# Kernel tuning notes

Measured on AMD Instinct MI355X. Metric: run time of the kernel, lower is better.

Reference implementation:

```python
import jax, jax.numpy as jnp
import numpy as np

B, S, H, E, I, K = 1, 4096, 1024, 16, 512, 2
ISH = 1024  # shared expert intermediate = moe_intermediate_size * num_shared_experts
ROUTE_SCALE = 1.0
WSCALE = 0.02


def setup_inputs() -> dict:
    key = jax.random.key(0)
    ks = jax.random.split(key, 9)
    return {
        "hidden_states": jax.random.normal(ks[0], (B, S, H), dtype=jnp.float32),
        "router_w": jax.random.normal(ks[1], (H, E), dtype=jnp.float32) * WSCALE,
        "expert_bias": jnp.zeros((E,), dtype=jnp.float32),
        "w_gate": jax.random.normal(ks[2], (E, H, I), dtype=jnp.float32) * WSCALE,
        "w_up": jax.random.normal(ks[3], (E, H, I), dtype=jnp.float32) * WSCALE,
        "w_down": jax.random.normal(ks[4], (E, I, H), dtype=jnp.float32) * WSCALE,
        "sw_gate": jax.random.normal(ks[5], (H, ISH), dtype=jnp.float32) * WSCALE,
        "sw_up": jax.random.normal(ks[6], (H, ISH), dtype=jnp.float32) * WSCALE,
        "sw_down": jax.random.normal(ks[7], (ISH, H), dtype=jnp.float32) * WSCALE,
    }


def reference(hidden_states, router_w, expert_bias, w_gate, w_up, w_down, sw_gate, sw_up, sw_down):
    b, s, h = hidden_states.shape
    T = b * s
    xf = hidden_states.reshape(T, h)

    # --- token-choice router (sigmoid scores, top-k, normalize, scale) ---
    scores = jax.nn.sigmoid((xf @ router_w).astype(jnp.float32))          # [T, E]
    _, sel = jax.lax.top_k(scores + expert_bias[None, :], K)              # [T, K] int32
    top = jnp.take_along_axis(scores, sel, axis=1)                        # [T, K]
    top = top / (top.sum(axis=-1, keepdims=True) + 1e-20)
    top = top * ROUTE_SCALE

    # combine weights: [T, E], zero for unselected experts
    comb = jnp.zeros((T, E), jnp.float32).at[jnp.arange(T)[:, None], sel].add(top)

    # --- routed experts: SwiGLU MLP per expert (stacked weights) ---
    g = jnp.einsum('th,ehi->eti', xf, w_gate)                             # [E, T, I]
    u = jnp.einsum('th,ehi->eti', xf, w_up)                               # [E, T, I]
    a = jax.nn.silu(g) * u                                                # [E, T, I]
    eo = jnp.einsum('eti,eih->eth', a, w_down)                            # [E, T, H]
    routed = jnp.einsum('eth,te->th', eo.astype(jnp.float32), comb).astype(hidden_states.dtype)

    # --- shared experts (always active) ---
    shared = (jax.nn.silu(xf @ sw_gate) * (xf @ sw_up)) @ sw_down         # [T, H]

    return (shared + routed).reshape(b, s, h)
```

## Files before the change

kernel.cpp:

```cpp
#include <hip/hip_runtime.h>
#include <math.h>

#define T_TOK 4096
#define HDIM  1024
#define NEXP  16
#define IDIM  512
#define NSLOT 16384
#define NGRP  18
#define MAXRB 160

typedef unsigned int u32;
typedef unsigned short u16;
typedef __attribute__((ext_vector_type(8))) short bfrag;
typedef __attribute__((ext_vector_type(4))) float f32x4;

__device__ __forceinline__ u16 f2bf(float f) {
    union { float f; u32 u; } c; c.f = f;
    u32 u = c.u;
    u32 r = u + 0x7fffu + ((u >> 16) & 1u);
    return (u16)(r >> 16);
}
__device__ __forceinline__ float bf2f(u16 h) {
    union { u32 u; float f; } c; c.u = ((u32)h) << 16;
    return c.f;
}

__device__ __forceinline__ void async16(void* lds, const void* g) {
    __builtin_amdgcn_global_load_lds((__attribute__((address_space(1))) void*)(g),
                                     (__attribute__((address_space(3))) void*)(lds),
                                     16, 0, 0);
}

#define SYNCN(n) do { \
    asm volatile("s_waitcnt vmcnt(" #n ")" ::: "memory"); \
    __builtin_amdgcn_s_barrier(); \
    __builtin_amdgcn_sched_barrier(0); \
} while (0)
#define BAR2() do { \
    __builtin_amdgcn_s_barrier(); \
    __builtin_amdgcn_sched_barrier(0); \
} while (0)

__global__ __launch_bounds__(256)
void transpose_all_k(const float* __restrict__ wg, const float* __restrict__ wu,
                     const float* __restrict__ wd, const float* __restrict__ swg,
                     const float* __restrict__ swu, const float* __restrict__ swd,
                     u16* __restrict__ WtG, u16* __restrict__ WtU, u16* __restrict__ WtD,
                     u16* __restrict__ SWtG, u16* __restrict__ SWtU, u16* __restrict__ SWtD) {
    int z = blockIdx.z;
    const float* src; u16* dst; int R, C; long base;
    if (z < 16)      { src = wg;  dst = WtG;  R = HDIM; C = IDIM;     base = (long)z * HDIM * IDIM; }
    else if (z < 32) { src = wu;  dst = WtU;  R = HDIM; C = IDIM;     base = (long)(z - 16) * HDIM * IDIM; }
    else if (z < 48) { src = wd;  dst = WtD;  R = IDIM; C = HDIM;     base = (long)(z - 32) * IDIM * HDIM; }
    else if (z == 48){ src = swg; dst = SWtG; R = HDIM; C = 2 * IDIM; base = 0; }
    else if (z == 49){ src = swu; dst = SWtU; R = HDIM; C = 2 * IDIM; base = 0; }
    else             { src = swd; dst = SWtD; R = IDIM; C = HDIM;     base = (long)(z - 50) * IDIM * HDIM; }
    if ((int)blockIdx.x >= C / 32 || (int)blockIdx.y >= R / 128) return;

    __shared__ u16 tileT[32][132];
    int c0 = blockIdx.x * 32, r0 = blockIdx.y * 128;
    int t = threadIdx.x;
    int rr = t >> 3;
    int c4 = (t & 7) * 4;
#pragma unroll
    for (int p = 0; p < 4; ++p) {
        int r = p * 32 + rr;
        float4 v = *(const float4*)(src + base + (long)(r0 + r) * C + c0 + c4);
        tileT[c4 + 0][r] = f2bf(v.x);
        tileT[c4 + 1][r] = f2bf(v.y);
        tileT[c4 + 2][r] = f2bf(v.z);
        tileT[c4 + 3][r] = f2bf(v.w);
    }
    __syncthreads();
    int cc = t >> 5;
    int r4 = (t & 31) * 4;
#pragma unroll
    for (int q = 0; q < 4; ++q) {
        int c = q * 8 + cc;
        ushort4 o;
        o.x = tileT[c][r4]; o.y = tileT[c][r4 + 1];
        o.z = tileT[c][r4 + 2]; o.w = tileT[c][r4 + 3];
        *(ushort4*)(dst + base + (long)(c0 + c) * R + r0 + r4) = o;
    }
}

__global__ __launch_bounds__(256) void router_k(const float* __restrict__ x,
                                                const float* __restrict__ rw,
                                                const float* __restrict__ bias,
                                                int* __restrict__ sel,
                                                float* __restrict__ wts,
                                                u16* __restrict__ x_bf) {
    int tid = threadIdx.x;
    int wv = tid >> 6;
    int lane = tid & 63;
    int t = blockIdx.x * 4 + wv;

    const float4* xr4 = (const float4*)(x + (long)t * HDIM);
    ushort4* xb4 = (ushort4*)(x_bf + (long)t * HDIM);
#pragma unroll
    for (int j = 0; j < 4; ++j) {
        float4 v = xr4[lane + j * 64];
        ushort4 ov;
        ov.x = f2bf(v.x); ov.y = f2bf(v.y); ov.z = f2bf(v.z); ov.w = f2bf(v.w);
        xb4[lane + j * 64] = ov;
    }

    int e = lane & 15, hc = lane >> 4;
    const float* xr = x + (long)t * HDIM + hc * 256;
    const float* rp = rw + (long)hc * 256 * NEXP + e;
    float acc = 0.f;
#pragma unroll 4
    for (int i = 0; i < 64; ++i) {
        float4 xv = *(const float4*)(xr + i * 4);
        acc += xv.x * rp[(i * 4 + 0) * NEXP] + xv.y * rp[(i * 4 + 1) * NEXP]
             + xv.z * rp[(i * 4 + 2) * NEXP] + xv.w * rp[(i * 4 + 3) * NEXP];
    }
    acc += __shfl_down(acc, 16);
    acc += __shfl_down(acc, 32);
    float sc = 1.f / (1.f + __expf(-acc));
    float v = sc + bias[e];
    int i0 = -1, i1 = -1;
    float v0 = -1e30f, v1 = -1e30f, s0 = 0.f, s1 = 0.f;
#pragma unroll
    for (int j = 0; j < 16; ++j) {
        float vj = __shfl(v, j);
        float scj = __shfl(sc, j);
        if (vj > v0) { v1 = v0; i1 = i0; s1 = s0; v0 = vj; i0 = j; s0 = scj; }
        else if (vj > v1) { v1 = vj; i1 = j; s1 = scj; }
    }
    if (lane == 0) {
        float nrm = s0 + s1 + 1e-20f;
        sel[t * 2] = i0; sel[t * 2 + 1] = i1;
        wts[t * 2] = s0 / nrm; wts[t * 2 + 1] = s1 / nrm;
    }
}

__global__ __launch_bounds__(1024) void route_build_k(const int* __restrict__ sel,
                                                      int* __restrict__ offs,
                                                      int* __restrict__ rowmap,
                                                      int* __restrict__ invmap,
                                                      int* __restrict__ rbGroup,
                                                      int* __restrict__ rbRow0) {
    __shared__ int hist[NEXP];
    __shared__ int cur[NEXP];
    int tid = threadIdx.x;
    if (tid < NEXP) hist[tid] = 0;
    __syncthreads();
    for (int i = tid; i < T_TOK * 2; i += 1024)
        atomicAdd(&hist[sel[i]], 1);
    __syncthreads();
    if (tid == 0) {
        int a = 0;
        for (int g = 0; g < NEXP; ++g) { cur[g] = a; offs[g] = a; a += hist[g]; }
        offs[16] = 8192;
        offs[17] = 8192 + T_TOK;
        offs[18] = 8192 + 2 * T_TOK;
        int rb = 0;
        for (int g = 0; g < NGRP; ++g)
            for (int r0 = offs[g]; r0 < offs[g + 1]; r0 += 128) {
                rbGroup[rb] = g; rbRow0[rb] = r0; ++rb;
            }
        for (; rb < MAXRB; ++rb) rbGroup[rb] = -1;
    }
    __syncthreads();
    for (int i = tid; i < T_TOK * 2; i += 1024) {
        int g = sel[i];
        int slot = atomicAdd(&cur[g], 1);
        rowmap[slot] = i >> 1;
        invmap[i] = slot;
    }
    for (int i = tid; i < T_TOK; i += 1024) {
        rowmap[8192 + i] = i;
        rowmap[8192 + T_TOK + i] = i;
    }
}

__global__ __launch_bounds__(256)
void gemm_gu(const u16* __restrict__ A,
             const u16* __restrict__ WG,
             const u16* __restrict__ WU,
             const u16* __restrict__ SWG,
             const u16* __restrict__ SWU,
             u16* __restrict__ H,
             const int* __restrict__ offs,
             const int* __restrict__ rowmap,
             const int* __restrict__ rbGroup,
             const int* __restrict__ rbRow0) {
    int rb = blockIdx.y;
    int g = rbGroup[rb];
    if (g < 0) return;
    int row0 = rbRow0[rb];
    int mend = offs[g + 1];
    int col0 = blockIdx.x * 64;
    long wb = (long)((g < 16) ? g : (g - 16)) * IDIM * HDIM;
    const u16* Bg = (g < 16) ? WG + wb : SWG + wb;
    const u16* Bu = (g < 16) ? WU + wb : SWU + wb;

    __shared__ u16 sA[2][128 * 64];
    __shared__ u16 sBg[2][64 * 64];
    __shared__ u16 sBu[2][64 * 64];

    int tid = threadIdx.x;
    int lane = tid & 63;
    int w = tid >> 6;
    int wr = (w >> 1) * 64, wc = (w & 1) * 32;
    int lhi = lane >> 4, llo = lane & 15;
    int swz = llo & 7;

    const u16* pA[4]; int dA[4];
#pragma unroll
    for (int c = 0; c < 4; ++c) {
        int idx = c * 256 + tid;
        int r = idx >> 3, ch = idx & 7;
        int grow = row0 + r;
        int ar = rowmap[(grow < mend) ? grow : row0];
        pA[c] = A + (long)ar * HDIM + ((ch ^ (r & 7)) * 8);
        dA[c] = idx * 8;
    }
    const u16* pBg[2]; const u16* pBu[2]; int dB[2];
#pragma unroll
    for (int c = 0; c < 2; ++c) {
        int idx = c * 256 + tid;
        int r = idx >> 3, ch = idx & 7;
        long boff = (long)(col0 + r) * HDIM + ((ch ^ (r & 7)) * 8);
        pBg[c] = Bg + boff; pBu[c] = Bu + boff;
        dB[c] = idx * 8;
    }

    f32x4 accg[4][2], accu[4][2];
#pragma unroll
    for (int m = 0; m < 4; ++m)
#pragma unroll
        for (int n = 0; n < 2; ++n) {
            f32x4 z = {0.f, 0.f, 0.f, 0.f};
            accg[m][n] = z; accu[m][n] = z;
        }

    auto STAGE = [&](int buf) {
#pragma unroll
        for (int c = 0; c < 4; ++c) { async16(&sA[buf][dA[c]], pA[c]); pA[c] += 64; }
#pragma unroll
        for (int c = 0; c < 2; ++c) {
            async16(&sBg[buf][dB[c]], pBg[c]); pBg[c] += 64;
            async16(&sBu[buf][dB[c]], pBu[c]); pBu[c] += 64;
        }
    };
    auto COMPUTE = [&](int buf) {
#pragma unroll
        for (int kk = 0; kk < 2; ++kk) {
            int p = ((kk * 4 + lhi) ^ swz) * 8;
            bfrag a[4], bg[2], bu[2];
#pragma unroll
            for (int m = 0; m < 4; ++m)
                a[m] = *(const bfrag*)&sA[buf][(wr + m * 16 + llo) * 64 + p];
#pragma unroll
            for (int n = 0; n < 2; ++n) {
                bg[n] = *(const bfrag*)&sBg[buf][(wc + n * 16 + llo) * 64 + p];
                bu[n] = *(const bfrag*)&sBu[buf][(wc + n * 16 + llo) * 64 + p];
            }
#pragma unroll
            for (int m = 0; m < 4; ++m)
#pragma unroll
                for (int n = 0; n < 2; ++n) {
                    accg[m][n] = __builtin_amdgcn_mfma_f32_16x16x32_bf16(a[m], bg[n], accg[m][n], 0, 0, 0);
                    accu[m][n] = __builtin_amdgcn_mfma_f32_16x16x32_bf16(a[m], bu[n], accu[m][n], 0, 0, 0);
                }
        }
    };

    STAGE(0);
#pragma unroll 1
    for (int t = 0; t < 14; t += 2) {
        STAGE(1); SYNCN(8); COMPUTE(0); BAR2();
        STAGE(0); SYNCN(8); COMPUTE(1); BAR2();
    }
    STAGE(1); SYNCN(8); COMPUTE(0); BAR2();
    SYNCN(0); COMPUTE(1);

#pragma unroll
    for (int m = 0; m < 4; ++m) {
        int rbase = row0 + wr + m * 16 + lhi * 4;
#pragma unroll
        for (int n = 0; n < 2; ++n) {
            int col = col0 + wc + n * 16 + llo;
#pragma unroll
            for (int i = 0; i < 4; ++i) {
                int grow = rbase + i;
                if (grow >= mend) continue;
                float gv = accg[m][n][i], uv = accu[m][n][i];
                float hv = gv / (1.f + __expf(-gv)) * uv;
                H[(long)grow * IDIM + col] = f2bf(hv);
            }
        }
    }
}

__global__ __launch_bounds__(256)
void gemm_down(const u16* __restrict__ Hbuf,
               const u16* __restrict__ WD,
               const u16* __restrict__ SWD,
               u16* __restrict__ EO,
               const int* __restrict__ offs,
               const int* __restrict__ rbGroup,
               const int* __restrict__ rbRow0) {
    int rb = blockIdx.y;
    int g = rbGroup[rb];
    if (g < 0) return;
    int row0 = rbRow0[rb];
    int mend = offs[g + 1];
    int col0 = blockIdx.x * 128;
    long wb = (long)((g < 16) ? g : (g - 16)) * HDIM * IDIM;
    const u16* B = (g < 16) ? WD + wb : SWD + wb;

    __shared__ u16 sA[2][128 * 64];
    __shared__ u16 sB[2][128 * 64];

    int tid = threadIdx.x;
    int lane = tid & 63;
    int w = tid >> 6;
    int wr = (w >> 1) * 64, wc = (w & 1) * 64;
    int lhi = lane >> 4, llo = lane & 15;
    int swz = llo & 7;

    const u16* pA[4]; const u16* pB[4]; int dd[4];
#pragma unroll
    for (int c = 0; c < 4; ++c) {
        int idx = c * 256 + tid;
        int r = idx >> 3, ch = idx & 7;
        int grow = row0 + r;
        int ar = (grow < mend) ? grow : row0;
        int chs = (ch ^ (r & 7)) * 8;
        pA[c] = Hbuf + (long)ar * IDIM + chs;
        pB[c] = B + (long)(col0 + r) * IDIM + chs;
        dd[c] = idx * 8;
    }

    f32x4 acc[4][4];
#pragma unroll
    for (int m = 0; m < 4; ++m)
#pragma unroll
        for (int n = 0; n < 4; ++n) { f32x4 z = {0.f, 0.f, 0.f, 0.f}; acc[m][n] = z; }

    auto STAGE = [&](int buf) {
#pragma unroll
        for (int c = 0; c < 4; ++c) {
            async16(&sA[buf][dd[c]], pA[c]); pA[c] += 64;
            async16(&sB[buf][dd[c]], pB[c]); pB[c] += 64;
        }
    };
    auto COMPUTE = [&](int buf) {
#pragma unroll
        for (int kk = 0; kk < 2; ++kk) {
            int p = ((kk * 4 + lhi) ^ swz) * 8;
            bfrag a[4], b[4];
#pragma unroll
            for (int m = 0; m < 4; ++m)
                a[m] = *(const bfrag*)&sA[buf][(wr + m * 16 + llo) * 64 + p];
#pragma unroll
            for (int n = 0; n < 4; ++n)
                b[n] = *(const bfrag*)&sB[buf][(wc + n * 16 + llo) * 64 + p];
#pragma unroll
            for (int m = 0; m < 4; ++m)
#pragma unroll
                for (int n = 0; n < 4; ++n)
                    acc[m][n] = __builtin_amdgcn_mfma_f32_16x16x32_bf16(a[m], b[n], acc[m][n], 0, 0, 0);
        }
    };

    STAGE(0);
#pragma unroll 1
    for (int t = 0; t < 6; t += 2) {
        STAGE(1); SYNCN(8); COMPUTE(0); BAR2();
        STAGE(0); SYNCN(8); COMPUTE(1); BAR2();
    }
    STAGE(1); SYNCN(8); COMPUTE(0); BAR2();
    SYNCN(0); COMPUTE(1);

#pragma unroll
    for (int m = 0; m < 4; ++m) {
        int rbase = row0 + wr + m * 16 + lhi * 4;
#pragma unroll
        for (int n = 0; n < 4; ++n) {
            int col = col0 + wc + n * 16 + llo;
#pragma unroll
            for (int i = 0; i < 4; ++i) {
                int grow = rbase + i;
                if (grow >= mend) continue;
                EO[(long)grow * HDIM + col] = f2bf(acc[m][n][i]);
            }
        }
    }
}

__global__ __launch_bounds__(256) void combine_k(float* __restrict__ out,
                                                 const u16* __restrict__ eo,
                                                 const int* __restrict__ invmap,
                                                 const float* __restrict__ wts) {
    int t = blockIdx.x;
    int h = threadIdx.x * 4;
    int r0 = invmap[t * 2], r1 = invmap[t * 2 + 1];
    float w0 = wts[t * 2], w1 = wts[t * 2 + 1];
    int s0 = 8192 + t, s1 = 8192 + T_TOK + t;
    ushort4 a = *(const ushort4*)(eo + (long)r0 * HDIM + h);
    ushort4 b = *(const ushort4*)(eo + (long)r1 * HDIM + h);
    ushort4 c = *(const ushort4*)(eo + (long)s0 * HDIM + h);
    ushort4 d = *(const ushort4*)(eo + (long)s1 * HDIM + h);
    float4 o;
    o.x = w0 * bf2f(a.x) + w1 * bf2f(b.x) + bf2f(c.x) + bf2f(d.x);
    o.y = w0 * bf2f(a.y) + w1 * bf2f(b.y) + bf2f(c.y) + bf2f(d.y);
    o.z = w0 * bf2f(a.z) + w1 * bf2f(b.z) + bf2f(c.z) + bf2f(d.z);
    o.w = w0 * bf2f(a.w) + w1 * bf2f(b.w) + bf2f(c.w) + bf2f(d.w);
    *(float4*)(out + (long)t * HDIM + h) = o;
}

extern "C" void kernel_launch(void* const* d_in, const int* in_sizes, int n_in,
                              void* d_out, int out_size, void* d_ws, size_t ws_size,
                              hipStream_t stream) {
    const float* x    = (const float*)d_in[0];
    const float* rw   = (const float*)d_in[1];
    const float* bias = (const float*)d_in[2];
    const float* wg   = (const float*)d_in[3];
    const float* wu   = (const float*)d_in[4];
    const float* wd   = (const float*)d_in[5];
    const float* swg  = (const float*)d_in[6];
    const float* swu  = (const float*)d_in[7];
    const float* swd  = (const float*)d_in[8];
    float* out = (float*)d_out;

    char* ws = (char*)d_ws;
    size_t o = 0;
    auto alloc = [&](size_t bytes) -> void* {
        void* p = ws + o;
        o += (bytes + 255) & ~(size_t)255;
        return p;
    };
    u16* x_bf = (u16*)alloc((size_t)T_TOK * HDIM * 2);
    u16* WtG  = (u16*)alloc((size_t)NEXP * IDIM * HDIM * 2);
    u16* WtU  = (u16*)alloc((size_t)NEXP * IDIM * HDIM * 2);
    u16* WtD  = (u16*)alloc((size_t)NEXP * HDIM * IDIM * 2);
    u16* SWtG = (u16*)alloc((size_t)2 * IDIM * HDIM * 2);
    u16* SWtU = (u16*)alloc((size_t)2 * IDIM * HDIM * 2);
    u16* SWtD = (u16*)alloc((size_t)2 * HDIM * IDIM * 2);
    u16* Hbuf = (u16*)alloc((size_t)NSLOT * IDIM * 2);
    int*   sel     = (int*)alloc((size_t)T_TOK * 2 * 4);
    float* wts     = (float*)alloc((size_t)T_TOK * 2 * 4);
    int*   invmap  = (int*)alloc((size_t)T_TOK * 2 * 4);
    int*   rowmap  = (int*)alloc((size_t)NSLOT * 4);
    int*   offs    = (int*)alloc((NGRP + 1) * 4);
    int*   rbGroup = (int*)alloc(MAXRB * 4);
    int*   rbRow0  = (int*)alloc(MAXRB * 4);
    u16* EO = WtG;

    transpose_all_k<<<dim3(32, 8, 52), 256, 0, stream>>>(
        wg, wu, wd, swg, swu, swd, WtG, WtU, WtD, SWtG, SWtU, SWtD);

    router_k<<<dim3(T_TOK / 4), 256, 0, stream>>>(x, rw, bias, sel, wts, x_bf);

    route_build_k<<<dim3(1), 1024, 0, stream>>>(sel, offs, rowmap, invmap, rbGroup, rbRow0);

    gemm_gu<<<dim3(IDIM / 64, MAXRB), 256, 0, stream>>>(
        x_bf, WtG, WtU, SWtG, SWtU, Hbuf, offs, rowmap, rbGroup, rbRow0);

    gemm_down<<<dim3(HDIM / 128, MAXRB), 256, 0, stream>>>(
        Hbuf, WtD, SWtD, EO, offs, rbGroup, rbRow0);

    combine_k<<<dim3(T_TOK), 256, 0, stream>>>(out, EO, invmap, wts);
}
```

Measured before the change: 164.6 us.

## Fuse weight transpose with router into one prep kernel and remap GEMM block order

Merges the weight transpose/bf16 conversion kernel and the router kernel into a single launch with a flat 1D grid, so there is one fewer launch and the two independent jobs can run on the GPU at the same time. Both grouped GEMMs move to a 1D grid with a remapped block index, (b&7)*160+(b>>3). With this mapping, blocks that are adjacent in dispatch order land on different row-blocks spread across the grid instead of walking the columns of one row-block. That changes which blocks are resident together, which can affect L2 reuse and per-XCD locality on the MI355X. The added risk is that the new remap may weaken weight-tile reuse across column blocks.

```diff
diff --git a/kernel.cpp b/kernel.cpp
--- a/kernel.cpp
+++ b/kernel.cpp
@@ -41,24 +41,11 @@
     __builtin_amdgcn_sched_barrier(0); \
 } while (0)
 
-__global__ __launch_bounds__(256)
-void transpose_all_k(const float* __restrict__ wg, const float* __restrict__ wu,
-                     const float* __restrict__ wd, const float* __restrict__ swg,
-                     const float* __restrict__ swu, const float* __restrict__ swd,
-                     u16* __restrict__ WtG, u16* __restrict__ WtU, u16* __restrict__ WtD,
-                     u16* __restrict__ SWtG, u16* __restrict__ SWtU, u16* __restrict__ SWtD) {
-    int z = blockIdx.z;
-    const float* src; u16* dst; int R, C; long base;
-    if (z < 16)      { src = wg;  dst = WtG;  R = HDIM; C = IDIM;     base = (long)z * HDIM * IDIM; }
-    else if (z < 32) { src = wu;  dst = WtU;  R = HDIM; C = IDIM;     base = (long)(z - 16) * HDIM * IDIM; }
-    else if (z < 48) { src = wd;  dst = WtD;  R = IDIM; C = HDIM;     base = (long)(z - 32) * IDIM * HDIM; }
-    else if (z == 48){ src = swg; dst = SWtG; R = HDIM; C = 2 * IDIM; base = 0; }
-    else if (z == 49){ src = swu; dst = SWtU; R = HDIM; C = 2 * IDIM; base = 0; }
-    else             { src = swd; dst = SWtD; R = IDIM; C = HDIM;     base = (long)(z - 50) * IDIM * HDIM; }
-    if ((int)blockIdx.x >= C / 32 || (int)blockIdx.y >= R / 128) return;
-
+__device__ __forceinline__ void transpose_tile(const float* __restrict__ src,
+                                               u16* __restrict__ dst,
+                                               int R, int C, long base, int bx, int by) {
     __shared__ u16 tileT[32][132];
-    int c0 = blockIdx.x * 32, r0 = blockIdx.y * 128;
+    int c0 = bx * 32, r0 = by * 128;
     int t = threadIdx.x;
     int rr = t >> 3;
     int c4 = (t & 7) * 4;
@@ -84,16 +71,45 @@
     }
 }
 
-__global__ __launch_bounds__(256) void router_k(const float* __restrict__ x,
-                                                const float* __restrict__ rw,
-                                                const float* __restrict__ bias,
-                                                int* __restrict__ sel,
-                                                float* __restrict__ wts,
-                                                u16* __restrict__ x_bf) {
+__global__ __launch_bounds__(256)
+void prep_k(const float* __restrict__ x, const float* __restrict__ rw,
+            const float* __restrict__ bias,
+            const float* __restrict__ wg, const float* __restrict__ wu,
+            const float* __restrict__ wd, const float* __restrict__ swg,
+            const float* __restrict__ swu, const float* __restrict__ swd,
+            u16* __restrict__ WtG, u16* __restrict__ WtU, u16* __restrict__ WtD,
+            u16* __restrict__ SWtG, u16* __restrict__ SWtU, u16* __restrict__ SWtD,
+            int* __restrict__ sel, float* __restrict__ wts, u16* __restrict__ x_bf) {
+    int b = blockIdx.x;
+    if (b < 2048) {
+        int e = b >> 7, t = b & 127;
+        transpose_tile(wg, WtG, HDIM, IDIM, (long)e * HDIM * IDIM, t & 15, t >> 4);
+        return;
+    } else if (b < 4096) {
+        int bb = b - 2048, e = bb >> 7, t = bb & 127;
+        transpose_tile(wu, WtU, HDIM, IDIM, (long)e * HDIM * IDIM, t & 15, t >> 4);
+        return;
+    } else if (b < 6144) {
+        int bb = b - 4096, e = bb >> 7, t = bb & 127;
+        transpose_tile(wd, WtD, IDIM, HDIM, (long)e * IDIM * HDIM, t & 31, t >> 5);
+        return;
+    } else if (b < 6400) {
+        int t = b - 6144;
+        transpose_tile(swg, SWtG, HDIM, 2 * IDIM, 0, t & 31, t >> 5);
+        return;
+    } else if (b < 6656) {
+        int t = b - 6400;
+        transpose_tile(swu, SWtU, HDIM, 2 * IDIM, 0, t & 31, t >> 5);
+        return;
+    } else if (b < 6912) {
+        int t = b - 6656, z = t >> 7, tt = t & 127;
+        transpose_tile(swd, SWtD, IDIM, HDIM, (long)z * IDIM * HDIM, tt & 31, tt >> 5);
+        return;
+    }
     int tid = threadIdx.x;
     int wv = tid >> 6;
     int lane = tid & 63;
-    int t = blockIdx.x * 4 + wv;
+    int t = (b - 6912) * 4 + wv;
 
     const float4* xr4 = (const float4*)(x + (long)t * HDIM);
     ushort4* xb4 = (ushort4*)(x_bf + (long)t * HDIM);
@@ -186,12 +202,15 @@
              const int* __restrict__ rowmap,
              const int* __restrict__ rbGroup,
              const int* __restrict__ rbRow0) {
-    int rb = blockIdx.y;
+    int b = blockIdx.x;
+    int L = (b & 7) * 160 + (b >> 3);
+    int cb = L & 7;
+    int rb = L >> 3;
     int g = rbGroup[rb];
     if (g < 0) return;
     int row0 = rbRow0[rb];
     int mend = offs[g + 1];
-    int col0 = blockIdx.x * 64;
+    int col0 = cb * 64;
     long wb = (long)((g < 16) ? g : (g - 16)) * IDIM * HDIM;
     const u16* Bg = (g < 16) ? WG + wb : SWG + wb;
     const u16* Bu = (g < 16) ? WU + wb : SWU + wb;
@@ -303,12 +322,15 @@
                const int* __restrict__ offs,
                const int* __restrict__ rbGroup,
                const int* __restrict__ rbRow0) {
-    int rb = blockIdx.y;
+    int b = blockIdx.x;
+    int L = (b & 7) * 160 + (b >> 3);
+    int cb = L & 7;
+    int rb = L >> 3;
     int g = rbGroup[rb];
     if (g < 0) return;
     int row0 = rbRow0[rb];
     int mend = offs[g + 1];
-    int col0 = blockIdx.x * 128;
+    int col0 = cb * 128;
     long wb = (long)((g < 16) ? g : (g - 16)) * HDIM * IDIM;
     const u16* B = (g < 16) ? WD + wb : SWD + wb;
 
@@ -352,18 +374,18 @@
 #pragma unroll
         for (int kk = 0; kk < 2; ++kk) {
             int p = ((kk * 4 + lhi) ^ swz) * 8;
-            bfrag a[4], b[4];
+            bfrag a[4], b2[4];
 #pragma unroll
             for (int m = 0; m < 4; ++m)
                 a[m] = *(const bfrag*)&sA[buf][(wr + m * 16 + llo) * 64 + p];
 #pragma unroll
             for (int n = 0; n < 4; ++n)
-                b[n] = *(const bfrag*)&sB[buf][(wc + n * 16 + llo) * 64 + p];
+                b2[n] = *(const bfrag*)&sB[buf][(wc + n * 16 + llo) * 64 + p];
 #pragma unroll
             for (int m = 0; m < 4; ++m)
 #pragma unroll
                 for (int n = 0; n < 4; ++n)
-                    acc[m][n] = __builtin_amdgcn_mfma_f32_16x16x32_bf16(a[m], b[n], acc[m][n], 0, 0, 0);
+                    acc[m][n] = __builtin_amdgcn_mfma_f32_16x16x32_bf16(a[m], b2[n], acc[m][n], 0, 0, 0);
         }
     };
 
@@ -451,17 +473,16 @@
     int*   rbRow0  = (int*)alloc(MAXRB * 4);
     u16* EO = WtG;
 
-    transpose_all_k<<<dim3(32, 8, 52), 256, 0, stream>>>(
-        wg, wu, wd, swg, swu, swd, WtG, WtU, WtD, SWtG, SWtU, SWtD);
-
-    router_k<<<dim3(T_TOK / 4), 256, 0, stream>>>(x, rw, bias, sel, wts, x_bf);
+    prep_k<<<dim3(6912 + 1024), 256, 0, stream>>>(
+        x, rw, bias, wg, wu, wd, swg, swu, swd,
+        WtG, WtU, WtD, SWtG, SWtU, SWtD, sel, wts, x_bf);
 
     route_build_k<<<dim3(1), 1024, 0, stream>>>(sel, offs, rowmap, invmap, rbGroup, rbRow0);
 
-    gemm_gu<<<dim3(IDIM / 64, MAXRB), 256, 0, stream>>>(
+    gemm_gu<<<dim3(8 * MAXRB), 256, 0, stream>>>(
         x_bf, WtG, WtU, SWtG, SWtU, Hbuf, offs, rowmap, rbGroup, rbRow0);
 
-    gemm_down<<<dim3(HDIM / 128, MAXRB), 256, 0, stream>>>(
+    gemm_down<<<dim3(8 * MAXRB), 256, 0, stream>>>(
         Hbuf, WtD, SWtD, EO, offs, rbGroup, rbRow0);
 
     combine_k<<<dim3(T_TOK), 256, 0, stream>>>(out, EO, invmap, wts);
```

Result: faster. 158.3 us (-3.8%).
